# Kernel optimization log

Hardware: AMD Instinct MI355X
Metric: run time of the kernel (lower is better)

The kernel has to match this reference:

```python
import jax, jax.numpy as jnp
import numpy as np

NEG = -65504.0
D = 640


def _linear(x, W, b):
    return x @ W + b


def _qkv_attention(q, k, v, mask4):
    # q:[B,Lq,D] k,v:[B,Lk,D] mask4:[B,1,1,Lk] (True = masked)
    scores = jnp.einsum('bqd,bkd->bqk', q, k) / jnp.sqrt(jnp.asarray(q.shape[-1], q.dtype))
    scores = jnp.where(mask4[:, 0, :, :], NEG, scores)  # mask.squeeze(1) -> [B,1,Lk]
    p = jax.nn.softmax(scores, axis=-1)
    return jnp.einsum('bqk,bkd->bqd', p, v)


def _attflat(x, mask4, W1, b1, W2, b2, Wm, bm):
    # x:[B,N,D]; glimpses == 1
    att = _linear(jax.nn.relu(_linear(x, W1, b1)), W2, b2)  # [B,N,1]
    m = mask4[:, 0, 0, :, None]                              # [B,N,1]
    att = jnp.where(m, NEG, att)
    att = jax.nn.softmax(att, axis=1)
    pooled = jnp.sum(att * x, axis=1)                        # [B,D]
    return _linear(pooled, Wm, bm), att[..., 0]              # att.squeeze() -> [B,N]


def setup_inputs() -> dict:
    key = jax.random.key(0)
    ks = jax.random.split(key, 16)
    B, Ni, Nq = 64, 512, 128
    s = 0.02
    inp = {
        'i_batch': jax.random.normal(ks[0], (B, Ni, D), jnp.float32),
        'q_batch': jax.random.normal(ks[1], (B, Nq, D), jnp.float32),
        'i_mask': jax.random.bernoulli(ks[2], 0.3, (B, 1, 1, Ni)),
        'q_mask': jax.random.bernoulli(ks[3], 0.3, (B, 1, 1, Nq)),
        # l_flatten params (applied to image-side features)
        'lW1': jax.random.normal(ks[4], (D, 2 * D), jnp.float32) * s,
        'lb1': jnp.zeros((2 * D,), jnp.float32),
        'lW2': jax.random.normal(ks[5], (2 * D, 1), jnp.float32) * s,
        'lb2': jnp.zeros((1,), jnp.float32),
        'lWm': jax.random.normal(ks[6], (D, D), jnp.float32) * s,
        'lbm': jnp.zeros((D,), jnp.float32),
        # i_flatten params (applied to language-side features)
        'iW1': jax.random.normal(ks[7], (D, 2 * D), jnp.float32) * s,
        'ib1': jnp.zeros((2 * D,), jnp.float32),
        'iW2': jax.random.normal(ks[8], (2 * D, 1), jnp.float32) * s,
        'ib2': jnp.zeros((1,), jnp.float32),
        'iWm': jax.random.normal(ks[9], (D, D), jnp.float32) * s,
        'ibm': jnp.zeros((D,), jnp.float32),
    }
    return inp


def reference(i_batch, q_batch, i_mask, q_mask,
              lW1, lb1, lW2, lb2, lWm, lbm,
              iW1, ib1, iW2, ib2, iWm, ibm):
    # image attends over question tokens
    i_feat = _qkv_attention(i_batch, q_batch, q_batch, q_mask)   # [B,Ni,D]
    i_feat, i_weight = _attflat(i_feat, i_mask, lW1, lb1, lW2, lb2, lWm, lbm)
    # question attends over image regions
    l_feat = _qkv_attention(q_batch, i_batch, i_batch, i_mask)   # [B,Nq,D]
    l_feat, _ = _attflat(l_feat, q_mask, iW1, ib1, iW2, ib2, iWm, ibm)
    return (i_feat, l_feat, i_weight)
```

## Files before the change

kernel.cpp:

```cpp
#include <hip/hip_runtime.h>
#include <cstdint>

#define DEV __device__ __forceinline__

typedef __attribute__((ext_vector_type(8))) short bf16x8;
typedef __attribute__((ext_vector_type(4))) float f32x4;

static constexpr int B  = 64;
static constexpr int NI = 512;
static constexpr int NQ = 128;
static constexpr int D  = 640;
static constexpr int H  = 1280;
static constexpr float NEGV  = -65504.0f;
static constexpr float SCALE = 0.039528470752104745f;

DEV unsigned short f2bf(float f) {
  union { float f; uint32_t u; } c; c.f = f;
  uint32_t u = c.u;
  u += 0x7fffu + ((u >> 16) & 1u);
  return (unsigned short)(u >> 16);
}
DEV float bf2f(unsigned short h) {
  union { uint32_t u; float f; } c; c.u = ((uint32_t)h) << 16;
  return c.f;
}

DEV void gll16(const void* g, void* l) {
  __builtin_amdgcn_global_load_lds(
      (const __attribute__((address_space(1))) void*)(uintptr_t)g,
      (__attribute__((address_space(3))) void*)(uint32_t)(uintptr_t)l,
      16, 0, 0);
}

DEV void stage_tile(const unsigned short* src, int ld, unsigned short* lds, int tid) {
  const int w = tid >> 6, lane = tid & 63;
#pragma unroll
  for (int i = 0; i < 2; ++i) {
    int c = w * 128 + i * 64 + lane;
    int r = c >> 2, kc = (c & 3) << 3;
    gll16(src + (long)r * ld + kc, (char*)lds + (size_t)c * 16);
  }
}

template<int OUT_BF16>
__global__ __launch_bounds__(256, 2) void gemm_nt(
    const unsigned short* __restrict__ A, const unsigned short* __restrict__ Bt,
    void* __restrict__ C, int lda, int ldb, int ldc, int K,
    long sA, long sB, long sC)
{
  __shared__ __align__(16) unsigned short lsA[128 * 32];
  __shared__ __align__(16) unsigned short lsB[128 * 32];
  const int tid = threadIdx.x;
  const int w = tid >> 6, lane = tid & 63;
  const int wm = w >> 1, wn = w & 1;
  const int g = lane >> 4, r = lane & 15;
  const long zb = blockIdx.z;
  const unsigned short* Ab = A + zb * sA + (long)blockIdx.x * 128 * lda;
  const unsigned short* Bb = Bt + zb * sB + (long)blockIdx.y * 128 * ldb;

  f32x4 acc[4][4] = {};
  for (int k0 = 0; k0 < K; k0 += 32) {
    stage_tile(Ab + k0, lda, lsA, tid);
    stage_tile(Bb + k0, ldb, lsB, tid);
    __syncthreads();
    bf16x8 af[4], bfr[4];
#pragma unroll
    for (int mi = 0; mi < 4; ++mi)
      af[mi] = *(const bf16x8*)&lsA[(wm * 64 + mi * 16 + r) * 32 + g * 8];
#pragma unroll
    for (int ni = 0; ni < 4; ++ni)
      bfr[ni] = *(const bf16x8*)&lsB[(wn * 64 + ni * 16 + r) * 32 + g * 8];
#pragma unroll
    for (int mi = 0; mi < 4; ++mi)
#pragma unroll
      for (int ni = 0; ni < 4; ++ni)
        acc[mi][ni] = __builtin_amdgcn_mfma_f32_16x16x32_bf16(af[mi], bfr[ni], acc[mi][ni], 0, 0, 0);
    __syncthreads();
  }
  const int row0 = blockIdx.x * 128 + wm * 64;
  const int col0 = blockIdx.y * 128 + wn * 64;
#pragma unroll
  for (int mi = 0; mi < 4; ++mi)
#pragma unroll
    for (int ni = 0; ni < 4; ++ni)
#pragma unroll
      for (int j = 0; j < 4; ++j) {
        int rr = row0 + mi * 16 + g * 4 + j;
        int cc = col0 + ni * 16 + r;
        float v = acc[mi][ni][j];
        if (OUT_BF16)
          ((unsigned short*)C)[zb * sC + (long)rr * ldc + cc] = f2bf(v);
        else
          ((float*)C)[zb * sC + (long)rr * ldc + cc] = v;
      }
}

__global__ __launch_bounds__(256, 2) void hatt_k(
    const unsigned short* __restrict__ A, const unsigned short* __restrict__ Bt,
    const float* __restrict__ b1, const float* __restrict__ W2,
    float* __restrict__ outlogit)
{
  __shared__ __align__(16) unsigned short lsA[128 * 32];
  __shared__ __align__(16) unsigned short lsB[128 * 32];
  __shared__ float b1c[128], w2c[128];
  const int tid = threadIdx.x;
  const int w = tid >> 6, lane = tid & 63;
  const int wm = w >> 1, wn = w & 1;
  const int g = lane >> 4, r = lane & 15;
  const int m0 = blockIdx.x * 128;
  const int n0 = blockIdx.y * 128;
  if (tid < 128) { b1c[tid] = b1[n0 + tid]; w2c[tid] = W2[n0 + tid]; }
  const unsigned short* Ab = A + (long)m0 * D;
  const unsigned short* Bb = Bt + (long)n0 * D;

  f32x4 acc[4][4] = {};
  for (int k0 = 0; k0 < D; k0 += 32) {
    stage_tile(Ab + k0, D, lsA, tid);
    stage_tile(Bb + k0, D, lsB, tid);
    __syncthreads();
    bf16x8 af[4], bfr[4];
#pragma unroll
    for (int mi = 0; mi < 4; ++mi)
      af[mi] = *(const bf16x8*)&lsA[(wm * 64 + mi * 16 + r) * 32 + g * 8];
#pragma unroll
    for (int ni = 0; ni < 4; ++ni)
      bfr[ni] = *(const bf16x8*)&lsB[(wn * 64 + ni * 16 + r) * 32 + g * 8];
#pragma unroll
    for (int mi = 0; mi < 4; ++mi)
#pragma unroll
      for (int ni = 0; ni < 4; ++ni)
        acc[mi][ni] = __builtin_amdgcn_mfma_f32_16x16x32_bf16(af[mi], bfr[ni], acc[mi][ni], 0, 0, 0);
    __syncthreads();
  }
  float rs[4][4];
#pragma unroll
  for (int mi = 0; mi < 4; ++mi)
#pragma unroll
    for (int j = 0; j < 4; ++j) rs[mi][j] = 0.f;
#pragma unroll
  for (int mi = 0; mi < 4; ++mi)
#pragma unroll
    for (int ni = 0; ni < 4; ++ni)
#pragma unroll
      for (int j = 0; j < 4; ++j) {
        int cl = wn * 64 + ni * 16 + r;
        float h = acc[mi][ni][j] + b1c[cl];
        h = fmaxf(h, 0.f);
        rs[mi][j] += h * w2c[cl];
      }
#pragma unroll
  for (int mi = 0; mi < 4; ++mi)
#pragma unroll
    for (int j = 0; j < 4; ++j) {
      float v = rs[mi][j];
      v += __shfl_xor(v, 1); v += __shfl_xor(v, 2);
      v += __shfl_xor(v, 4); v += __shfl_xor(v, 8);
      if (r == 0) atomicAdd(&outlogit[m0 + wm * 64 + mi * 16 + g * 4 + j], v);
    }
}

template<int L>
__global__ void sm_scores(const float* __restrict__ S, const int* __restrict__ mask,
                          unsigned short* __restrict__ P, int M)
{
  constexpr int NV = L / 64;
  const int wid = threadIdx.x >> 6, lane = threadIdx.x & 63;
  const long row = (long)blockIdx.x * 4 + wid;
  const int b = (int)(row / M);
  const float* s = S + row * (long)L;
  const int* mk = mask + (long)b * L;
  float x[NV];
  float mx = -__builtin_inff();
#pragma unroll
  for (int i = 0; i < NV; ++i) {
    int idx = i * 64 + lane;
    float v = s[idx] * SCALE;
    x[i] = mk[idx] ? NEGV : v;
    mx = fmaxf(mx, x[i]);
  }
#pragma unroll
  for (int sft = 32; sft >= 1; sft >>= 1) mx = fmaxf(mx, __shfl_xor(mx, sft));
  float sum = 0.f;
#pragma unroll
  for (int i = 0; i < NV; ++i) { x[i] = __expf(x[i] - mx); sum += x[i]; }
#pragma unroll
  for (int sft = 32; sft >= 1; sft >>= 1) sum += __shfl_xor(sum, sft);
  const float inv = 1.f / sum;
  unsigned short* p = P + row * (long)L;
#pragma unroll
  for (int i = 0; i < NV; ++i) p[i * 64 + lane] = f2bf(x[i] * inv);
}

template<int L>
__global__ void sm_att(const float* __restrict__ logit, const int* __restrict__ mask,
                       const float* __restrict__ b2p, float* __restrict__ att,
                       float* __restrict__ iw)
{
  constexpr int PER = (L + 255) / 256;
  __shared__ float red[4];
  const int tid = threadIdx.x, b = blockIdx.x;
  const float b2v = b2p[0];
  float xs[PER];
  float mx = -__builtin_inff();
#pragma unroll
  for (int i = 0; i < PER; ++i) {
    int idx = tid + i * 256;
    if (idx < L) {
      float v = mask[(long)b * L + idx] ? NEGV : (logit[(long)b * L + idx] + b2v);
      xs[i] = v; mx = fmaxf(mx, v);
    } else xs[i] = -__builtin_inff();
  }
#pragma unroll
  for (int s = 32; s >= 1; s >>= 1) mx = fmaxf(mx, __shfl_xor(mx, s));
  if ((tid & 63) == 0) red[tid >> 6] = mx;
  __syncthreads();
  mx = fmaxf(fmaxf(red[0], red[1]), fmaxf(red[2], red[3]));
  __syncthreads();
  float sum = 0.f;
#pragma unroll
  for (int i = 0; i < PER; ++i) {
    int idx = tid + i * 256;
    if (idx < L) { xs[i] = __expf(xs[i] - mx); sum += xs[i]; }
  }
#pragma unroll
  for (int s = 32; s >= 1; s >>= 1) sum += __shfl_xor(sum, s);
  if ((tid & 63) == 0) red[tid >> 6] = sum;
  __syncthreads();
  sum = red[0] + red[1] + red[2] + red[3];
  const float inv = 1.f / sum;
#pragma unroll
  for (int i = 0; i < PER; ++i) {
    int idx = tid + i * 256;
    if (idx < L) {
      float a = xs[i] * inv;
      att[(long)b * L + idx] = a;
      if (iw) iw[(long)b * L + idx] = a;
    }
  }
}

template<int L>
__global__ void pooled_k(const float* __restrict__ att, const unsigned short* __restrict__ X,
                         float* __restrict__ out)
{
  __shared__ float a[L];
  const int b = blockIdx.x, tid = threadIdx.x;
  const int d = blockIdx.y * 128 + tid;
  for (int i = tid; i < L; i += 128) a[i] = att[(long)b * L + i];
  __syncthreads();
  const unsigned short* xb = X + (long)b * L * D + d;
  float acc = 0.f;
#pragma unroll 4
  for (int m = 0; m < L; ++m) acc += a[m] * bf2f(xb[(long)m * D]);
  out[b * D + d] = acc;
}

__global__ void final_k(const float* __restrict__ pooled, const float* __restrict__ W,
                        const float* __restrict__ bias, float* __restrict__ out)
{
  __shared__ float p[D];
  const int b = blockIdx.x, tid = threadIdx.x;
  const int nn = blockIdx.y * 128 + tid;
  for (int i = tid; i < D; i += 128) p[i] = pooled[b * D + i];
  __syncthreads();
  float acc = bias[nn];
  for (int k = 0; k < D; ++k) acc += p[k] * W[(long)k * D + nn];
  out[b * D + nn] = acc;
}

__global__ void cast_bf_k(const float* __restrict__ in, unsigned short* __restrict__ out, long n4)
{
  const long i = (long)blockIdx.x * 256 + threadIdx.x;
  if (i < n4) {
    const float4 v = ((const float4*)in)[i];
    unsigned short* op = out + i * 4;
    op[0] = f2bf(v.x); op[1] = f2bf(v.y); op[2] = f2bf(v.z); op[3] = f2bf(v.w);
  }
}

__global__ void tcast_k(const float* __restrict__ in, unsigned short* __restrict__ out, int R, int C)
{
  __shared__ float t[32][33];
  const int tx = threadIdx.x, ty = threadIdx.y;
  const long base = (long)blockIdx.z * R * C;
  const float* ib = in + base;
  unsigned short* ob = out + base;
  const int c0 = blockIdx.x * 32, r0 = blockIdx.y * 32;
#pragma unroll
  for (int k = 0; k < 4; ++k)
    t[ty + k * 8][tx] = ib[(long)(r0 + ty + k * 8) * C + c0 + tx];
  __syncthreads();
#pragma unroll
  for (int k = 0; k < 4; ++k)
    ob[(long)(c0 + ty + k * 8) * R + r0 + tx] = f2bf(t[tx][ty + k * 8]);
}

extern "C" void kernel_launch(void* const* d_in, const int* in_sizes, int n_in,
                              void* d_out, int out_size, void* d_ws, size_t ws_size,
                              hipStream_t stream)
{
  (void)in_sizes; (void)n_in; (void)out_size; (void)ws_size;
  const float* i_batch = (const float*)d_in[0];
  const float* q_batch = (const float*)d_in[1];
  const int*   i_mask  = (const int*)d_in[2];
  const int*   q_mask  = (const int*)d_in[3];
  const float* lW1 = (const float*)d_in[4];
  const float* lb1 = (const float*)d_in[5];
  const float* lW2 = (const float*)d_in[6];
  const float* lb2 = (const float*)d_in[7];
  const float* lWm = (const float*)d_in[8];
  const float* lbm = (const float*)d_in[9];
  const float* iW1 = (const float*)d_in[10];
  const float* ib1 = (const float*)d_in[11];
  const float* iW2 = (const float*)d_in[12];
  const float* ib2 = (const float*)d_in[13];
  const float* iWm = (const float*)d_in[14];
  const float* ibm = (const float*)d_in[15];
  float* out_if = (float*)d_out;
  float* out_lf = out_if + B * D;
  float* out_iw = out_lf + B * D;

  char* wp = (char*)d_ws;
  size_t off = 0;
  auto alloc = [&](size_t bytes) { void* p = wp + off; off += (bytes + 255) & ~(size_t)255; return p; };
  unsigned short* i_bf   = (unsigned short*)alloc((size_t)B * NI * D * 2);
  unsigned short* q_bf   = (unsigned short*)alloc((size_t)B * NQ * D * 2);
  unsigned short* x1_bf  = (unsigned short*)alloc((size_t)B * NI * D * 2);
  unsigned short* q_bfT  = (unsigned short*)alloc((size_t)B * NQ * D * 2);
  float*          scores = (float*)alloc((size_t)B * NI * NQ * 4);
  unsigned short* p_bf   = (unsigned short*)alloc((size_t)B * NI * NQ * 2);
  unsigned short* lW1t   = (unsigned short*)alloc((size_t)H * D * 2);
  unsigned short* iW1t   = (unsigned short*)alloc((size_t)H * D * 2);
  float* logit1  = (float*)alloc((size_t)B * NI * 4);
  float* att1    = (float*)alloc((size_t)B * NI * 4);
  float* logit2  = (float*)alloc((size_t)B * NQ * 4);
  float* att2    = (float*)alloc((size_t)B * NQ * 4);
  float* pooled1 = (float*)alloc((size_t)B * D * 4);
  float* pooled2 = (float*)alloc((size_t)B * D * 4);
  unsigned short* i_bfT = x1_bf;
  unsigned short* x2_bf = q_bfT;

  cast_bf_k<<<dim3((unsigned)((long)B * NI * D / 4 / 256)), 256, 0, stream>>>(i_batch, i_bf, (long)B * NI * D / 4);
  cast_bf_k<<<dim3((unsigned)((long)B * NQ * D / 4 / 256)), 256, 0, stream>>>(q_batch, q_bf, (long)B * NQ * D / 4);
  tcast_k<<<dim3(D / 32, NQ / 32, B), dim3(32, 8), 0, stream>>>(q_batch, q_bfT, NQ, D);
  tcast_k<<<dim3(H / 32, D / 32, 1), dim3(32, 8), 0, stream>>>(lW1, lW1t, D, H);
  tcast_k<<<dim3(H / 32, D / 32, 1), dim3(32, 8), 0, stream>>>(iW1, iW1t, D, H);

  gemm_nt<0><<<dim3(NI / 128, NQ / 128, B), 256, 0, stream>>>(
      i_bf, q_bf, scores, D, D, NQ, D, (long)NI * D, (long)NQ * D, (long)NI * NQ);
  sm_scores<NQ><<<dim3(B * NI / 4), 256, 0, stream>>>(scores, q_mask, p_bf, NI);
  gemm_nt<1><<<dim3(NI / 128, D / 128, B), 256, 0, stream>>>(
      p_bf, q_bfT, x1_bf, NQ, NQ, D, NQ, (long)NI * NQ, (long)D * NQ, (long)NI * D);
  hipMemsetAsync(logit1, 0, (size_t)B * NI * 4, stream);
  hatt_k<<<dim3(B * NI / 128, H / 128), 256, 0, stream>>>(x1_bf, lW1t, lb1, lW2, logit1);
  sm_att<NI><<<dim3(B), 256, 0, stream>>>(logit1, i_mask, lb2, att1, out_iw);
  pooled_k<NI><<<dim3(B, D / 128), 128, 0, stream>>>(att1, x1_bf, pooled1);
  final_k<<<dim3(B, D / 128), 128, 0, stream>>>(pooled1, lWm, lbm, out_if);

  tcast_k<<<dim3(D / 32, NI / 32, B), dim3(32, 8), 0, stream>>>(i_batch, i_bfT, NI, D);
  gemm_nt<0><<<dim3(NQ / 128, NI / 128, B), 256, 0, stream>>>(
      q_bf, i_bf, scores, D, D, NI, D, (long)NQ * D, (long)NI * D, (long)NQ * NI);
  sm_scores<NI><<<dim3(B * NQ / 4), 256, 0, stream>>>(scores, i_mask, p_bf, NQ);
  gemm_nt<1><<<dim3(NQ / 128, D / 128, B), 256, 0, stream>>>(
      p_bf, i_bfT, x2_bf, NI, NI, D, NI, (long)NQ * NI, (long)D * NI, (long)NQ * D);
  hipMemsetAsync(logit2, 0, (size_t)B * NQ * 4, stream);
  hatt_k<<<dim3(B * NQ / 128, H / 128), 256, 0, stream>>>(x2_bf, iW1t, ib1, iW2, logit2);
  sm_att<NQ><<<dim3(B), 256, 0, stream>>>(logit2, q_mask, ib2, att2, nullptr);
  pooled_k<NQ><<<dim3(B, D / 128), 128, 0, stream>>>(att2, x2_bf, pooled2);
  final_k<<<dim3(B, D / 128), 128, 0, stream>>>(pooled2, iWm, ibm, out_lf);
}
```

Baseline: 497.8 us.

## Deepen GEMM K-tile with swizzled LDS, fuse casts, split pooling and final reductions

GEMM and hidden-attention kernels now stage 64-wide K tiles into XOR-swizzled LDS, which halves the barrier count and avoids bank conflicts. The hatt grid is reordered so consecutive blocks share the same A rows. The cast and transpose of the inputs are fused into one kernel that writes both layouts, so each input is read once. pooled_k splits the sequence across four wave groups and final_k splits K across z-blocks with atomicAdd onto a pre-zeroed output, adding parallelism at the cost of atomics and more LDS per block.

```diff
diff --git a/kernel.cpp b/kernel.cpp
--- a/kernel.cpp
+++ b/kernel.cpp
@@ -32,14 +32,19 @@
       16, 0, 0);
 }
 
-DEV void stage_tile(const unsigned short* src, int ld, unsigned short* lds, int tid) {
+DEV void stage64(const unsigned short* src, int ld, unsigned short* lds, int tid) {
   const int w = tid >> 6, lane = tid & 63;
 #pragma unroll
-  for (int i = 0; i < 2; ++i) {
-    int c = w * 128 + i * 64 + lane;
-    int r = c >> 2, kc = (c & 3) << 3;
-    gll16(src + (long)r * ld + kc, (char*)lds + (size_t)c * 16);
-  }
+  for (int i = 0; i < 4; ++i) {
+    int c = w * 256 + i * 64 + lane;
+    int r = c >> 3, ck = c & 7;
+    int col8 = ((ck ^ (r & 7)) << 3);
+    gll16(src + (long)r * ld + col8, (char*)lds + (size_t)c * 16);
+  }
+}
+
+DEV bf16x8 frag(const unsigned short* ls, int row, int q) {
+  return *(const bf16x8*)&ls[row * 64 + (((q ^ (row & 7))) << 3)];
 }
 
 template<int OUT_BF16>
@@ -48,8 +53,8 @@
     void* __restrict__ C, int lda, int ldb, int ldc, int K,
     long sA, long sB, long sC)
 {
-  __shared__ __align__(16) unsigned short lsA[128 * 32];
-  __shared__ __align__(16) unsigned short lsB[128 * 32];
+  __shared__ __align__(16) unsigned short lsA[128 * 64];
+  __shared__ __align__(16) unsigned short lsB[128 * 64];
   const int tid = threadIdx.x;
   const int w = tid >> 6, lane = tid & 63;
   const int wm = w >> 1, wn = w & 1;
@@ -59,22 +64,23 @@
   const unsigned short* Bb = Bt + zb * sB + (long)blockIdx.y * 128 * ldb;
 
   f32x4 acc[4][4] = {};
-  for (int k0 = 0; k0 < K; k0 += 32) {
-    stage_tile(Ab + k0, lda, lsA, tid);
-    stage_tile(Bb + k0, ldb, lsB, tid);
+  for (int k0 = 0; k0 < K; k0 += 64) {
+    stage64(Ab + k0, lda, lsA, tid);
+    stage64(Bb + k0, ldb, lsB, tid);
     __syncthreads();
-    bf16x8 af[4], bfr[4];
-#pragma unroll
-    for (int mi = 0; mi < 4; ++mi)
-      af[mi] = *(const bf16x8*)&lsA[(wm * 64 + mi * 16 + r) * 32 + g * 8];
-#pragma unroll
-    for (int ni = 0; ni < 4; ++ni)
-      bfr[ni] = *(const bf16x8*)&lsB[(wn * 64 + ni * 16 + r) * 32 + g * 8];
-#pragma unroll
-    for (int mi = 0; mi < 4; ++mi)
-#pragma unroll
-      for (int ni = 0; ni < 4; ++ni)
-        acc[mi][ni] = __builtin_amdgcn_mfma_f32_16x16x32_bf16(af[mi], bfr[ni], acc[mi][ni], 0, 0, 0);
+#pragma unroll
+    for (int kk = 0; kk < 2; ++kk) {
+      bf16x8 af[4], bfr[4];
+#pragma unroll
+      for (int mi = 0; mi < 4; ++mi) af[mi]  = frag(lsA, wm * 64 + mi * 16 + r, kk * 4 + g);
+#pragma unroll
+      for (int ni = 0; ni < 4; ++ni) bfr[ni] = frag(lsB, wn * 64 + ni * 16 + r, kk * 4 + g);
+#pragma unroll
+      for (int mi = 0; mi < 4; ++mi)
+#pragma unroll
+        for (int ni = 0; ni < 4; ++ni)
+          acc[mi][ni] = __builtin_amdgcn_mfma_f32_16x16x32_bf16(af[mi], bfr[ni], acc[mi][ni], 0, 0, 0);
+    }
     __syncthreads();
   }
   const int row0 = blockIdx.x * 128 + wm * 64;
@@ -100,36 +106,37 @@
     const float* __restrict__ b1, const float* __restrict__ W2,
     float* __restrict__ outlogit)
 {
-  __shared__ __align__(16) unsigned short lsA[128 * 32];
-  __shared__ __align__(16) unsigned short lsB[128 * 32];
+  __shared__ __align__(16) unsigned short lsA[128 * 64];
+  __shared__ __align__(16) unsigned short lsB[128 * 64];
   __shared__ float b1c[128], w2c[128];
   const int tid = threadIdx.x;
   const int w = tid >> 6, lane = tid & 63;
   const int wm = w >> 1, wn = w & 1;
   const int g = lane >> 4, r = lane & 15;
-  const int m0 = blockIdx.x * 128;
-  const int n0 = blockIdx.y * 128;
+  const int n0 = blockIdx.x * 128;
+  const int m0 = blockIdx.y * 128;
   if (tid < 128) { b1c[tid] = b1[n0 + tid]; w2c[tid] = W2[n0 + tid]; }
   const unsigned short* Ab = A + (long)m0 * D;
   const unsigned short* Bb = Bt + (long)n0 * D;
 
   f32x4 acc[4][4] = {};
-  for (int k0 = 0; k0 < D; k0 += 32) {
-    stage_tile(Ab + k0, D, lsA, tid);
-    stage_tile(Bb + k0, D, lsB, tid);
+  for (int k0 = 0; k0 < D; k0 += 64) {
+    stage64(Ab + k0, D, lsA, tid);
+    stage64(Bb + k0, D, lsB, tid);
     __syncthreads();
-    bf16x8 af[4], bfr[4];
-#pragma unroll
-    for (int mi = 0; mi < 4; ++mi)
-      af[mi] = *(const bf16x8*)&lsA[(wm * 64 + mi * 16 + r) * 32 + g * 8];
-#pragma unroll
-    for (int ni = 0; ni < 4; ++ni)
-      bfr[ni] = *(const bf16x8*)&lsB[(wn * 64 + ni * 16 + r) * 32 + g * 8];
-#pragma unroll
-    for (int mi = 0; mi < 4; ++mi)
-#pragma unroll
-      for (int ni = 0; ni < 4; ++ni)
-        acc[mi][ni] = __builtin_amdgcn_mfma_f32_16x16x32_bf16(af[mi], bfr[ni], acc[mi][ni], 0, 0, 0);
+#pragma unroll
+    for (int kk = 0; kk < 2; ++kk) {
+      bf16x8 af[4], bfr[4];
+#pragma unroll
+      for (int mi = 0; mi < 4; ++mi) af[mi]  = frag(lsA, wm * 64 + mi * 16 + r, kk * 4 + g);
+#pragma unroll
+      for (int ni = 0; ni < 4; ++ni) bfr[ni] = frag(lsB, wn * 64 + ni * 16 + r, kk * 4 + g);
+#pragma unroll
+      for (int mi = 0; mi < 4; ++mi)
+#pragma unroll
+        for (int ni = 0; ni < 4; ++ni)
+          acc[mi][ni] = __builtin_amdgcn_mfma_f32_16x16x32_bf16(af[mi], bfr[ni], acc[mi][ni], 0, 0, 0);
+    }
     __syncthreads();
   }
   float rs[4][4];
@@ -244,47 +251,65 @@
                          float* __restrict__ out)
 {
   __shared__ float a[L];
+  __shared__ float part[4][64];
   const int b = blockIdx.x, tid = threadIdx.x;
-  const int d = blockIdx.y * 128 + tid;
-  for (int i = tid; i < L; i += 128) a[i] = att[(long)b * L + i];
+  const int dcol = tid & 63, grp = tid >> 6;
+  const int d = blockIdx.y * 64 + dcol;
+  for (int i = tid; i < L; i += 256) a[i] = att[(long)b * L + i];
   __syncthreads();
   const unsigned short* xb = X + (long)b * L * D + d;
   float acc = 0.f;
+  const int m0 = grp * (L / 4);
 #pragma unroll 4
-  for (int m = 0; m < L; ++m) acc += a[m] * bf2f(xb[(long)m * D]);
-  out[b * D + d] = acc;
+  for (int m = m0; m < m0 + L / 4; ++m) acc += a[m] * bf2f(xb[(long)m * D]);
+  part[grp][dcol] = acc;
+  __syncthreads();
+  if (tid < 64)
+    out[b * D + blockIdx.y * 64 + tid] = part[0][tid] + part[1][tid] + part[2][tid] + part[3][tid];
 }
 
 __global__ void final_k(const float* __restrict__ pooled, const float* __restrict__ W,
                         const float* __restrict__ bias, float* __restrict__ out)
 {
-  __shared__ float p[D];
+  __shared__ float p[160];
   const int b = blockIdx.x, tid = threadIdx.x;
   const int nn = blockIdx.y * 128 + tid;
-  for (int i = tid; i < D; i += 128) p[i] = pooled[b * D + i];
-  __syncthreads();
-  float acc = bias[nn];
-  for (int k = 0; k < D; ++k) acc += p[k] * W[(long)k * D + nn];
-  out[b * D + nn] = acc;
-}
-
-__global__ void cast_bf_k(const float* __restrict__ in, unsigned short* __restrict__ out, long n4)
-{
-  const long i = (long)blockIdx.x * 256 + threadIdx.x;
-  if (i < n4) {
-    const float4 v = ((const float4*)in)[i];
-    unsigned short* op = out + i * 4;
-    op[0] = f2bf(v.x); op[1] = f2bf(v.y); op[2] = f2bf(v.z); op[3] = f2bf(v.w);
-  }
-}
-
-__global__ void tcast_k(const float* __restrict__ in, unsigned short* __restrict__ out, int R, int C)
+  const int k0 = blockIdx.z * 160;
+  for (int i = tid; i < 160; i += 128) p[i] = pooled[b * D + k0 + i];
+  __syncthreads();
+  float acc = (blockIdx.z == 0) ? bias[nn] : 0.f;
+  for (int k = 0; k < 160; ++k) acc += p[k] * W[(long)(k0 + k) * D + nn];
+  atomicAdd(&out[b * D + nn], acc);
+}
+
+__global__ void cast_t_k(const float* __restrict__ in, unsigned short* __restrict__ outN,
+                         unsigned short* __restrict__ outT, int R, int C)
 {
   __shared__ float t[32][33];
   const int tx = threadIdx.x, ty = threadIdx.y;
   const long base = (long)blockIdx.z * R * C;
   const float* ib = in + base;
-  unsigned short* ob = out + base;
+  unsigned short* obN = outN + base;
+  unsigned short* obT = outT + base;
+  const int c0 = blockIdx.x * 32, r0 = blockIdx.y * 32;
+#pragma unroll
+  for (int k = 0; k < 4; ++k) {
+    float v = ib[(long)(r0 + ty + k * 8) * C + c0 + tx];
+    t[ty + k * 8][tx] = v;
+    obN[(long)(r0 + ty + k * 8) * C + c0 + tx] = f2bf(v);
+  }
+  __syncthreads();
+#pragma unroll
+  for (int k = 0; k < 4; ++k)
+    obT[(long)(c0 + ty + k * 8) * R + r0 + tx] = f2bf(t[tx][ty + k * 8]);
+}
+
+__global__ void tcast_k(const float* __restrict__ in, unsigned short* __restrict__ out, int R, int C)
+{
+  __shared__ float t[32][33];
+  const int tx = threadIdx.x, ty = threadIdx.y;
+  const float* ib = in;
+  unsigned short* ob = out;
   const int c0 = blockIdx.x * 32, r0 = blockIdx.y * 32;
 #pragma unroll
   for (int k = 0; k < 4; ++k)
@@ -324,9 +349,11 @@
   size_t off = 0;
   auto alloc = [&](size_t bytes) { void* p = wp + off; off += (bytes + 255) & ~(size_t)255; return p; };
   unsigned short* i_bf   = (unsigned short*)alloc((size_t)B * NI * D * 2);
+  unsigned short* i_bfT  = (unsigned short*)alloc((size_t)B * NI * D * 2);
   unsigned short* q_bf   = (unsigned short*)alloc((size_t)B * NQ * D * 2);
+  unsigned short* q_bfT  = (unsigned short*)alloc((size_t)B * NQ * D * 2);
   unsigned short* x1_bf  = (unsigned short*)alloc((size_t)B * NI * D * 2);
-  unsigned short* q_bfT  = (unsigned short*)alloc((size_t)B * NQ * D * 2);
+  unsigned short* x2_bf  = (unsigned short*)alloc((size_t)B * NQ * D * 2);
   float*          scores = (float*)alloc((size_t)B * NI * NQ * 4);
   unsigned short* p_bf   = (unsigned short*)alloc((size_t)B * NI * NQ * 2);
   unsigned short* lW1t   = (unsigned short*)alloc((size_t)H * D * 2);
@@ -337,35 +364,33 @@
   float* att2    = (float*)alloc((size_t)B * NQ * 4);
   float* pooled1 = (float*)alloc((size_t)B * D * 4);
   float* pooled2 = (float*)alloc((size_t)B * D * 4);
-  unsigned short* i_bfT = x1_bf;
-  unsigned short* x2_bf = q_bfT;
-
-  cast_bf_k<<<dim3((unsigned)((long)B * NI * D / 4 / 256)), 256, 0, stream>>>(i_batch, i_bf, (long)B * NI * D / 4);
-  cast_bf_k<<<dim3((unsigned)((long)B * NQ * D / 4 / 256)), 256, 0, stream>>>(q_batch, q_bf, (long)B * NQ * D / 4);
-  tcast_k<<<dim3(D / 32, NQ / 32, B), dim3(32, 8), 0, stream>>>(q_batch, q_bfT, NQ, D);
-  tcast_k<<<dim3(H / 32, D / 32, 1), dim3(32, 8), 0, stream>>>(lW1, lW1t, D, H);
-  tcast_k<<<dim3(H / 32, D / 32, 1), dim3(32, 8), 0, stream>>>(iW1, iW1t, D, H);
+
+  hipMemsetAsync(out_if, 0, (size_t)2 * B * D * 4, stream);
+  hipMemsetAsync(logit1, 0, (size_t)B * NI * 4, stream);
+  hipMemsetAsync(logit2, 0, (size_t)B * NQ * 4, stream);
+
+  cast_t_k<<<dim3(D / 32, NI / 32, B), dim3(32, 8), 0, stream>>>(i_batch, i_bf, i_bfT, NI, D);
+  cast_t_k<<<dim3(D / 32, NQ / 32, B), dim3(32, 8), 0, stream>>>(q_batch, q_bf, q_bfT, NQ, D);
+  tcast_k<<<dim3(H / 32, D / 32), dim3(32, 8), 0, stream>>>(lW1, lW1t, D, H);
+  tcast_k<<<dim3(H / 32, D / 32), dim3(32, 8), 0, stream>>>(iW1, iW1t, D, H);
 
   gemm_nt<0><<<dim3(NI / 128, NQ / 128, B), 256, 0, stream>>>(
       i_bf, q_bf, scores, D, D, NQ, D, (long)NI * D, (long)NQ * D, (long)NI * NQ);
   sm_scores<NQ><<<dim3(B * NI / 4), 256, 0, stream>>>(scores, q_mask, p_bf, NI);
   gemm_nt<1><<<dim3(NI / 128, D / 128, B), 256, 0, stream>>>(
       p_bf, q_bfT, x1_bf, NQ, NQ, D, NQ, (long)NI * NQ, (long)D * NQ, (long)NI * D);
-  hipMemsetAsync(logit1, 0, (size_t)B * NI * 4, stream);
-  hatt_k<<<dim3(B * NI / 128, H / 128), 256, 0, stream>>>(x1_bf, lW1t, lb1, lW2, logit1);
+  hatt_k<<<dim3(H / 128, B * NI / 128), 256, 0, stream>>>(x1_bf, lW1t, lb1, lW2, logit1);
   sm_att<NI><<<dim3(B), 256, 0, stream>>>(logit1, i_mask, lb2, att1, out_iw);
-  pooled_k<NI><<<dim3(B, D / 128), 128, 0, stream>>>(att1, x1_bf, pooled1);
-  final_k<<<dim3(B, D / 128), 128, 0, stream>>>(pooled1, lWm, lbm, out_if);
-
-  tcast_k<<<dim3(D / 32, NI / 32, B), dim3(32, 8), 0, stream>>>(i_batch, i_bfT, NI, D);
+  pooled_k<NI><<<dim3(B, D / 64), 256, 0, stream>>>(att1, x1_bf, pooled1);
+  final_k<<<dim3(B, D / 128, 4), 128, 0, stream>>>(pooled1, lWm, lbm, out_if);
+
   gemm_nt<0><<<dim3(NQ / 128, NI / 128, B), 256, 0, stream>>>(
       q_bf, i_bf, scores, D, D, NI, D, (long)NQ * D, (long)NI * D, (long)NQ * NI);
   sm_scores<NI><<<dim3(B * NQ / 4), 256, 0, stream>>>(scores, i_mask, p_bf, NQ);
   gemm_nt<1><<<dim3(NQ / 128, D / 128, B), 256, 0, stream>>>(
       p_bf, i_bfT, x2_bf, NI, NI, D, NI, (long)NQ * NI, (long)D * NI, (long)NQ * D);
-  hipMemsetAsync(logit2, 0, (size_t)B * NQ * 4, stream);
-  hatt_k<<<dim3(B * NQ / 128, H / 128), 256, 0, stream>>>(x2_bf, iW1t, ib1, iW2, logit2);
+  hatt_k<<<dim3(H / 128, B * NQ / 128), 256, 0, stream>>>(x2_bf, iW1t, ib1, iW2, logit2);
   sm_att<NQ><<<dim3(B), 256, 0, stream>>>(logit2, q_mask, ib2, att2, nullptr);
-  pooled_k<NQ><<<dim3(B, D / 128), 128, 0, stream>>>(att2, x2_bf, pooled2);
-  final_k<<<dim3(B, D / 128), 128, 0, stream>>>(pooled2, iWm, ibm, out_lf);
-}
+  pooled_k<NQ><<<dim3(B, D / 64), 256, 0, stream>>>(att2, x2_bf, pooled2);
+  final_k<<<dim3(B, D / 128, 4), 128, 0, stream>>>(pooled2, iWm, ibm, out_lf);
+}
```

Measured after the change: 434.0 us. 1.15x faster.
